# Kernel tuning notes

Hardware: AMD Instinct MI355X
Metric: run time of the kernel (lower is better)

## Reference

```python
import jax, jax.numpy as jnp
import numpy as np

NUM_CLASSES = 100
CLUSTERS_PER_CLASS = 64
LATENT_DIM = 128
BATCH = 32768


def setup_inputs() -> dict:
    key = jax.random.key(0)
    kx, kc, kl = jax.random.split(key, 3)
    x = jax.random.normal(kx, (BATCH, LATENT_DIM), dtype=jnp.float32)
    # nn.Parameter(torch.randn(C, Kc, D) * 0.1)
    centers = jax.random.normal(kc, (NUM_CLASSES, CLUSTERS_PER_CLASS, LATENT_DIM), dtype=jnp.float32) * 0.1
    labels = jax.random.randint(kl, (BATCH,), 0, NUM_CLASSES, dtype=jnp.int64)
    return {"x": x, "centers": centers, "labels": labels}


def reference(x, centers, labels):
    # [C, Kc, D] -> [K, D]
    all_centers = centers.reshape(-1, LATENT_DIM).astype(x.dtype)
    x2 = jnp.sum(x * x, axis=-1, keepdims=True)            # [B,1]
    c2 = jnp.sum(all_centers * all_centers, axis=-1)       # [K]
    sq = x2 + c2[None, :] - 2.0 * jnp.einsum('bd,kd->bk', x, all_centers)
    distances = jnp.sqrt(jnp.maximum(sq, 0.0))             # [B,K]
    closest_indices = jnp.argmin(distances, axis=1)        # [B]
    class_predictions = closest_indices // CLUSTERS_PER_CLASS
    cluster_assignments = closest_indices % CLUSTERS_PER_CLASS
    quantized_hard = all_centers[closest_indices]          # [B,D]
    min_distances = jnp.take_along_axis(distances, closest_indices[:, None], axis=1)[:, 0]
    # straight-through estimator (training path in the torch module)
    quantized = x + jax.lax.stop_gradient(quantized_hard - x)
    return quantized, cluster_assignments, min_distances, class_predictions
```

## Files before the change

kernel.cpp:

```cpp
#include <hip/hip_runtime.h>
#include <math.h>

#define BATCH  32768
#define D      128
#define K      6400
#define KC     64
#define ROWS_PER_BLOCK 64
#define CHUNK_C 128
#define NCHUNKS 50

typedef _Float16 half8 __attribute__((ext_vector_type(8)));
typedef float    floatx4 __attribute__((ext_vector_type(4)));

typedef __attribute__((address_space(3))) unsigned       lds_uint;
typedef __attribute__((address_space(1))) const unsigned glb_uint;

__device__ __forceinline__ void async_lds16(const void* g, void* l) {
    __builtin_amdgcn_global_load_lds((glb_uint*)g, (lds_uint*)l, 16, 0, 0);
}

__global__ __launch_bounds__(256) void pack_kernel(const float* __restrict__ centers,
                                                   _Float16* __restrict__ wh,
                                                   float* __restrict__ c2n) {
    int tid = blockIdx.x * 256 + threadIdx.x;
    int ch = tid >> 11;
    int u  = (tid >> 7) & 15;
    int cw = tid & 127;
    int center = ch * CHUNK_C + cw;
    const float* src = centers + (size_t)center * D + u * 8;
    float4 a = *(const float4*)src;
    float4 b = *(const float4*)(src + 4);
    float f[8] = {a.x, a.y, a.z, a.w, b.x, b.y, b.z, b.w};
    half8 h;
#pragma unroll
    for (int j = 0; j < 8; ++j) h[j] = (_Float16)f[j];
    *(half8*)(wh + (size_t)tid * 8) = h;

    if (blockIdx.x < K / KC) {
        int c_local = threadIdx.x >> 2, part = threadIdx.x & 3;
        int c = blockIdx.x * 64 + c_local;
        const float4* p = (const float4*)(centers + (size_t)c * D + part * 32);
        float s = 0.f;
#pragma unroll
        for (int i = 0; i < 8; ++i) {
            float4 v = p[i];
            s = fmaf(v.x, v.x, s); s = fmaf(v.y, v.y, s);
            s = fmaf(v.z, v.z, s); s = fmaf(v.w, v.w, s);
        }
        s += __shfl_xor(s, 1, 64);
        s += __shfl_xor(s, 2, 64);
        if (part == 0) c2n[c] = -0.5f * s;
    }
}

__global__ __launch_bounds__(512, 4) void dist_kernel(
    const float* __restrict__ x, const float* __restrict__ centers,
    const _Float16* __restrict__ wh, const float* __restrict__ c2n,
    float* __restrict__ out) {
    __shared__ char lds[65536];

    const int t    = threadIdx.x;
    const int w    = t >> 6;
    const int L    = t & 63;
    const int quad = L >> 4;
    const int n16  = L & 15;
    const int cq   = w & 3;
    const int rq   = w >> 2;
    const int gr0  = blockIdx.x * ROWS_PER_BLOCK;

    half8 Ah[2][4];
#pragma unroll
    for (int rt = 0; rt < 2; ++rt) {
        int r = gr0 + rq * 32 + rt * 16 + n16;
        const float* xr = x + (size_t)r * D + quad * 8;
#pragma unroll
        for (int ks = 0; ks < 4; ++ks) {
            float4 a = *(const float4*)(xr + ks * 32);
            float4 b = *(const float4*)(xr + ks * 32 + 4);
            float f[8] = {a.x, a.y, a.z, a.w, b.x, b.y, b.z, b.w};
            half8 h;
#pragma unroll
            for (int j = 0; j < 8; ++j) h[j] = (_Float16)f[j];
            Ah[rt][ks] = h;
        }
    }

    float b1[8], b2[8];
    int   j1_[8], j2_[8];
#pragma unroll
    for (int k = 0; k < 8; ++k) { b1[k] = -3.4e38f; b2[k] = -3.4e38f; j1_[k] = 0; j2_[k] = 0; }

    float pv[8]; int pi[8];
#pragma unroll
    for (int k = 0; k < 8; ++k) { pv[k] = -3.4e38f; pi[k] = 0; }

    const char* gh = (const char*)wh;

#pragma unroll
    for (int i = 0; i < 4; ++i) {
        int seg = w + i * 8;
        async_lds16(gh + seg * 1024 + L * 16, lds + seg * 1024);
    }

    float c2vA[2], c2vB[2];
#pragma unroll
    for (int ct = 0; ct < 2; ++ct) c2vA[ct] = c2n[cq * 32 + ct * 16 + n16];
    __syncthreads();

    for (int ci = 0; ci < NCHUNKS; ++ci) {
        const char* cur = lds + (ci & 1) * 32768;
        if (ci + 1 < NCHUNKS) {
            const char* gn = gh + (size_t)(ci + 1) * 32768;
            char* nxt = lds + ((ci + 1) & 1) * 32768;
#pragma unroll
            for (int i = 0; i < 4; ++i) {
                int seg = w + i * 8;
                async_lds16(gn + seg * 1024 + L * 16, nxt + seg * 1024);
            }
            const int kb1 = (ci + 1) * CHUNK_C + cq * 32;
#pragma unroll
            for (int ct = 0; ct < 2; ++ct) c2vB[ct] = c2n[kb1 + ct * 16 + n16];
        }

#pragma unroll
        for (int k = 0; k < 8; ++k) {
            float v = pv[k]; int vi = pi[k];
            bool bet1 = v > b1[k];
            bool bet2 = v > b2[k];
            float nb2 = bet1 ? b1[k] : (bet2 ? v : b2[k]);
            int   nj2 = bet1 ? j1_[k] : (bet2 ? vi : j2_[k]);
            b1[k]  = bet1 ? v : b1[k];
            j1_[k] = bet1 ? vi : j1_[k];
            b2[k]  = nb2;
            j2_[k] = nj2;
        }

        const int kbase = ci * CHUNK_C + cq * 32;

        floatx4 acc[2][2];
#pragma unroll
        for (int rt = 0; rt < 2; ++rt)
#pragma unroll
            for (int ct = 0; ct < 2; ++ct)
                acc[rt][ct] = (floatx4){c2vA[ct], c2vA[ct], c2vA[ct], c2vA[ct]};

        __builtin_amdgcn_s_setprio(1);
#pragma unroll
        for (int ks = 0; ks < 4; ++ks) {
            const half8* pb = (const half8*)cur + (ks * 4 + quad) * 128 + cq * 32 + n16;
#pragma unroll
            for (int ct = 0; ct < 2; ++ct) {
                half8 Bf = pb[ct * 16];
                acc[0][ct] = __builtin_amdgcn_mfma_f32_16x16x32_f16(Ah[0][ks], Bf, acc[0][ct], 0, 0, 0);
                acc[1][ct] = __builtin_amdgcn_mfma_f32_16x16x32_f16(Ah[1][ks], Bf, acc[1][ct], 0, 0, 0);
            }
        }
        __builtin_amdgcn_s_setprio(0);

        int i0 = kbase + n16;
#pragma unroll
        for (int rt = 0; rt < 2; ++rt)
#pragma unroll
            for (int reg = 0; reg < 4; ++reg) {
                float s0 = acc[rt][0][reg], s1 = acc[rt][1][reg];
                bool g01 = s1 > s0;
                int k = rt * 4 + reg;
                pv[k] = g01 ? s1 : s0;
                pi[k] = g01 ? i0 + 16 : i0;
            }

#pragma unroll
        for (int ct = 0; ct < 2; ++ct) c2vA[ct] = c2vB[ct];

        __syncthreads();
    }

#pragma unroll
    for (int k = 0; k < 8; ++k) {
        float v = pv[k]; int vi = pi[k];
        bool bet1 = v > b1[k];
        bool bet2 = v > b2[k];
        float nb2 = bet1 ? b1[k] : (bet2 ? v : b2[k]);
        int   nj2 = bet1 ? j1_[k] : (bet2 ? vi : j2_[k]);
        b1[k]  = bet1 ? v : b1[k];
        j1_[k] = bet1 ? vi : j1_[k];
        b2[k]  = nb2;
        j2_[k] = nj2;
    }

    int* candL = (int*)lds;

#pragma unroll
    for (int k = 0; k < 8; ++k) {
        float v1 = b1[k], v2 = b2[k];
        int   p1 = j1_[k], p2 = j2_[k];
#pragma unroll
        for (int m = 1; m < 16; m <<= 1) {
            float o1 = __shfl_xor(v1, m, 64), o2 = __shfl_xor(v2, m, 64);
            int   q1 = __shfl_xor(p1, m, 64), q2 = __shfl_xor(p2, m, 64);
            bool firstMine = (v1 > o1) || (v1 == o1 && p1 < q1);
            float nv1 = firstMine ? v1 : o1;  int np1 = firstMine ? p1 : q1;
            float cb  = firstMine ? o1 : v1;  int cpi = firstMine ? q1 : p1;
            float ob  = firstMine ? v2 : o2;  int obi = firstMine ? p2 : q2;
            bool secOwn = (ob > cb) || (ob == cb && obi < cpi);
            v1 = nv1; p1 = np1;
            v2 = secOwn ? ob : cb;  p2 = secOwn ? obi : cpi;
        }
        if (n16 == 0) {
            int rloc = rq * 32 + (k >> 2) * 16 + quad * 4 + (k & 3);
            candL[rloc * 8 + cq * 2 + 0] = p1;
            candL[rloc * 8 + cq * 2 + 1] = p2;
        }
    }
    __syncthreads();

    {
        int r = t >> 3, p = t & 7;
        int row = gr0 + r;
        int ix = candL[r * 8 + p];
        const float4* xr4 = (const float4*)(x + (size_t)row * D);
        const float4* c4  = (const float4*)(centers + (size_t)ix * D);
        float dot = 0.f, x2s = 0.f, c2 = 0.f;
#pragma unroll
        for (int d4 = 0; d4 < 32; ++d4) {
            float4 xv = xr4[d4], cv = c4[d4];
            dot = fmaf(xv.x, cv.x, dot); dot = fmaf(xv.y, cv.y, dot);
            dot = fmaf(xv.z, cv.z, dot); dot = fmaf(xv.w, cv.w, dot);
            x2s = fmaf(xv.x, xv.x, x2s); x2s = fmaf(xv.y, xv.y, x2s);
            x2s = fmaf(xv.z, xv.z, x2s); x2s = fmaf(xv.w, xv.w, x2s);
            c2  = fmaf(cv.x, cv.x, c2);  c2  = fmaf(cv.y, cv.y, c2);
            c2  = fmaf(cv.z, cv.z, c2);  c2  = fmaf(cv.w, cv.w, c2);
        }
        float sq = x2s + c2 - 2.f * dot;
#pragma unroll
        for (int m = 1; m < 8; m <<= 1) {
            float osq = __shfl_xor(sq, m, 64);
            int   oix = __shfl_xor(ix, m, 64);
            if (osq < sq || (osq == sq && oix < ix)) { sq = osq; ix = oix; }
        }

        float* out_clu = out + (size_t)BATCH * D;
        float* out_md  = out_clu + BATCH;
        float* out_cls = out_md + BATCH;
        if (p == 0) {
            out_md[row]  = sqrtf(fmaxf(sq, 0.f));
            out_clu[row] = (float)(ix & (KC - 1));
            out_cls[row] = (float)(ix >> 6);
        }

        const float4* cv4 = (const float4*)(centers + (size_t)ix * D) + p * 4;
        const float4* xv4 = (const float4*)(x + (size_t)row * D) + p * 4;
        float4* o4 = (float4*)(out + (size_t)row * D) + p * 4;
#pragma unroll
        for (int i = 0; i < 4; ++i) {
            float4 cv = cv4[i], xv = xv4[i];
            float4 o;
            o.x = xv.x + (cv.x - xv.x);
            o.y = xv.y + (cv.y - xv.y);
            o.z = xv.z + (cv.z - xv.z);
            o.w = xv.w + (cv.w - xv.w);
            o4[i] = o;
        }
    }
}

extern "C" void kernel_launch(void* const* d_in, const int* in_sizes, int n_in,
                              void* d_out, int out_size, void* d_ws, size_t ws_size,
                              hipStream_t stream) {
    const float* x       = (const float*)d_in[0];
    const float* centers = (const float*)d_in[1];
    float* out = (float*)d_out;

    _Float16* wh  = (_Float16*)d_ws;
    float*    c2n = (float*)(wh + (size_t)K * D);

    pack_kernel<<<(K * 16) / 256, 256, 0, stream>>>(centers, wh, c2n);
    dist_kernel<<<BATCH / ROWS_PER_BLOCK, 512, 0, stream>>>(x, centers, wh, c2n, out);
}
```

Before: 189.6 us.

## Load center fragments directly into registers, dropping LDS double buffer

Replaces the LDS double-buffered async global-to-LDS staging of packed fp16 centers with direct per-wave global loads into register double buffers (B0/B1), unrolled by two chunks. This removes the per-chunk __syncthreads and LDS traffic, and the launch bounds drop to 2 blocks per CU to make room for the extra registers. The cost is that each wave in a block loads the same center data separately through L1/L2 instead of sharing it via LDS, and occupancy is lower.

```diff
diff --git a/kernel.cpp b/kernel.cpp
--- a/kernel.cpp
+++ b/kernel.cpp
@@ -11,13 +11,6 @@
 
 typedef _Float16 half8 __attribute__((ext_vector_type(8)));
 typedef float    floatx4 __attribute__((ext_vector_type(4)));
-
-typedef __attribute__((address_space(3))) unsigned       lds_uint;
-typedef __attribute__((address_space(1))) const unsigned glb_uint;
-
-__device__ __forceinline__ void async_lds16(const void* g, void* l) {
-    __builtin_amdgcn_global_load_lds((glb_uint*)g, (lds_uint*)l, 16, 0, 0);
-}
 
 __global__ __launch_bounds__(256) void pack_kernel(const float* __restrict__ centers,
                                                    _Float16* __restrict__ wh,
@@ -53,11 +46,67 @@
     }
 }
 
-__global__ __launch_bounds__(512, 4) void dist_kernel(
+#define INSERT_PV()                                                         \
+    _Pragma("unroll")                                                       \
+    for (int k = 0; k < 8; ++k) {                                           \
+        float v = pv[k]; int vi = pi[k];                                    \
+        bool bet1 = v > b1[k];                                              \
+        bool bet2 = v > b2[k];                                              \
+        float nb2 = bet1 ? b1[k] : (bet2 ? v : b2[k]);                      \
+        int   nj2 = bet1 ? j1_[k] : (bet2 ? vi : j2_[k]);                   \
+        b1[k]  = bet1 ? v : b1[k];                                          \
+        j1_[k] = bet1 ? vi : j1_[k];                                        \
+        b2[k]  = nb2;                                                       \
+        j2_[k] = nj2;                                                       \
+    }
+
+#define COMPUTE_CHUNK(Bx, c2x, ci_)                                         \
+    {                                                                       \
+        floatx4 acc[2][2];                                                  \
+        _Pragma("unroll")                                                   \
+        for (int rt = 0; rt < 2; ++rt)                                      \
+            _Pragma("unroll")                                               \
+            for (int ct = 0; ct < 2; ++ct)                                  \
+                acc[rt][ct] = (floatx4){c2x[ct], c2x[ct], c2x[ct], c2x[ct]};\
+        _Pragma("unroll")                                                   \
+        for (int ks = 0; ks < 4; ++ks) {                                    \
+            _Pragma("unroll")                                               \
+            for (int ct = 0; ct < 2; ++ct) {                                \
+                half8 Bf = Bx[ks * 2 + ct];                                 \
+                acc[0][ct] = __builtin_amdgcn_mfma_f32_16x16x32_f16(Ah[0][ks], Bf, acc[0][ct], 0, 0, 0); \
+                acc[1][ct] = __builtin_amdgcn_mfma_f32_16x16x32_f16(Ah[1][ks], Bf, acc[1][ct], 0, 0, 0); \
+            }                                                               \
+        }                                                                   \
+        int i0 = (ci_) * CHUNK_C + cq * 32 + n16;                           \
+        _Pragma("unroll")                                                   \
+        for (int rt = 0; rt < 2; ++rt)                                      \
+            _Pragma("unroll")                                               \
+            for (int reg = 0; reg < 4; ++reg) {                             \
+                float s0 = acc[rt][0][reg], s1 = acc[rt][1][reg];           \
+                bool g01 = s1 > s0;                                         \
+                int k = rt * 4 + reg;                                       \
+                pv[k] = g01 ? s1 : s0;                                      \
+                pi[k] = g01 ? i0 + 16 : i0;                                 \
+            }                                                               \
+    }
+
+#define LOAD_B(Bx, ci_)                                                     \
+    _Pragma("unroll")                                                       \
+    for (int ks = 0; ks < 4; ++ks)                                          \
+        _Pragma("unroll")                                                   \
+        for (int ct = 0; ct < 2; ++ct)                                      \
+            Bx[ks * 2 + ct] = gB[(size_t)(ci_) * 2048 + ks * 512 + ct * 16];
+
+#define LOAD_C2(c2x, ci_)                                                   \
+    _Pragma("unroll")                                                       \
+    for (int ct = 0; ct < 2; ++ct)                                          \
+        c2x[ct] = c2n[(ci_) * CHUNK_C + cq * 32 + ct * 16 + n16];
+
+__global__ __launch_bounds__(512, 2) void dist_kernel(
     const float* __restrict__ x, const float* __restrict__ centers,
     const _Float16* __restrict__ wh, const float* __restrict__ c2n,
     float* __restrict__ out) {
-    __shared__ char lds[65536];
+    __shared__ int candL[ROWS_PER_BLOCK * 8];
 
     const int t    = threadIdx.x;
     const int w    = t >> 6;
@@ -94,101 +143,29 @@
 #pragma unroll
     for (int k = 0; k < 8; ++k) { pv[k] = -3.4e38f; pi[k] = 0; }
 
-    const char* gh = (const char*)wh;
-
-#pragma unroll
-    for (int i = 0; i < 4; ++i) {
-        int seg = w + i * 8;
-        async_lds16(gh + seg * 1024 + L * 16, lds + seg * 1024);
-    }
-
-    float c2vA[2], c2vB[2];
-#pragma unroll
-    for (int ct = 0; ct < 2; ++ct) c2vA[ct] = c2n[cq * 32 + ct * 16 + n16];
-    __syncthreads();
-
-    for (int ci = 0; ci < NCHUNKS; ++ci) {
-        const char* cur = lds + (ci & 1) * 32768;
-        if (ci + 1 < NCHUNKS) {
-            const char* gn = gh + (size_t)(ci + 1) * 32768;
-            char* nxt = lds + ((ci + 1) & 1) * 32768;
-#pragma unroll
-            for (int i = 0; i < 4; ++i) {
-                int seg = w + i * 8;
-                async_lds16(gn + seg * 1024 + L * 16, nxt + seg * 1024);
-            }
-            const int kb1 = (ci + 1) * CHUNK_C + cq * 32;
-#pragma unroll
-            for (int ct = 0; ct < 2; ++ct) c2vB[ct] = c2n[kb1 + ct * 16 + n16];
-        }
-
-#pragma unroll
-        for (int k = 0; k < 8; ++k) {
-            float v = pv[k]; int vi = pi[k];
-            bool bet1 = v > b1[k];
-            bool bet2 = v > b2[k];
-            float nb2 = bet1 ? b1[k] : (bet2 ? v : b2[k]);
-            int   nj2 = bet1 ? j1_[k] : (bet2 ? vi : j2_[k]);
-            b1[k]  = bet1 ? v : b1[k];
-            j1_[k] = bet1 ? vi : j1_[k];
-            b2[k]  = nb2;
-            j2_[k] = nj2;
-        }
-
-        const int kbase = ci * CHUNK_C + cq * 32;
-
-        floatx4 acc[2][2];
-#pragma unroll
-        for (int rt = 0; rt < 2; ++rt)
-#pragma unroll
-            for (int ct = 0; ct < 2; ++ct)
-                acc[rt][ct] = (floatx4){c2vA[ct], c2vA[ct], c2vA[ct], c2vA[ct]};
-
-        __builtin_amdgcn_s_setprio(1);
-#pragma unroll
-        for (int ks = 0; ks < 4; ++ks) {
-            const half8* pb = (const half8*)cur + (ks * 4 + quad) * 128 + cq * 32 + n16;
-#pragma unroll
-            for (int ct = 0; ct < 2; ++ct) {
-                half8 Bf = pb[ct * 16];
-                acc[0][ct] = __builtin_amdgcn_mfma_f32_16x16x32_f16(Ah[0][ks], Bf, acc[0][ct], 0, 0, 0);
-                acc[1][ct] = __builtin_amdgcn_mfma_f32_16x16x32_f16(Ah[1][ks], Bf, acc[1][ct], 0, 0, 0);
-            }
-        }
-        __builtin_amdgcn_s_setprio(0);
-
-        int i0 = kbase + n16;
-#pragma unroll
-        for (int rt = 0; rt < 2; ++rt)
-#pragma unroll
-            for (int reg = 0; reg < 4; ++reg) {
-                float s0 = acc[rt][0][reg], s1 = acc[rt][1][reg];
-                bool g01 = s1 > s0;
-                int k = rt * 4 + reg;
-                pv[k] = g01 ? s1 : s0;
-                pi[k] = g01 ? i0 + 16 : i0;
-            }
-
-#pragma unroll
-        for (int ct = 0; ct < 2; ++ct) c2vA[ct] = c2vB[ct];
-
-        __syncthreads();
-    }
-
-#pragma unroll
-    for (int k = 0; k < 8; ++k) {
-        float v = pv[k]; int vi = pi[k];
-        bool bet1 = v > b1[k];
-        bool bet2 = v > b2[k];
-        float nb2 = bet1 ? b1[k] : (bet2 ? v : b2[k]);
-        int   nj2 = bet1 ? j1_[k] : (bet2 ? vi : j2_[k]);
-        b1[k]  = bet1 ? v : b1[k];
-        j1_[k] = bet1 ? vi : j1_[k];
-        b2[k]  = nb2;
-        j2_[k] = nj2;
-    }
-
-    int* candL = (int*)lds;
+    const half8* gB = (const half8*)wh + quad * 128 + cq * 32 + n16;
+
+    half8 B0[8], B1[8];
+    float c2A[2], c2B[2];
+
+    LOAD_B(B0, 0)
+    LOAD_C2(c2A, 0)
+
+    for (int cc = 0; cc < NCHUNKS; cc += 2) {
+        LOAD_B(B1, cc + 1)
+        LOAD_C2(c2B, cc + 1)
+        INSERT_PV()
+        COMPUTE_CHUNK(B0, c2A, cc)
+
+        if (cc + 2 < NCHUNKS) {
+            LOAD_B(B0, cc + 2)
+            LOAD_C2(c2A, cc + 2)
+        }
+        INSERT_PV()
+        COMPUTE_CHUNK(B1, c2B, cc + 1)
+    }
+
+    INSERT_PV()
 
 #pragma unroll
     for (int k = 0; k < 8; ++k) {
```

New measurement: 191.3 us. No clear change (+0.9%).

## Halve rows per block, drop LDS double buffering to raise occupancy

Applied to the files above, without the earlier changes.

Each block now handles 32 rows instead of 64. The 64KB double-buffered center staging becomes a single 32KB buffer that is loaded and then synchronized at each chunk, and the launch bound asks for 8 blocks per CU. The pending-value register pipeline is dropped and the top-2 update is folded directly into the MFMA epilogue, which cuts register pressure. The aim is to hide memory latency through more resident blocks rather than in-block prefetch, at the cost of an exposed load and barrier per chunk and twice as many blocks re-reading the centers. The final straight-through write is also re-split so all 512 threads write coalesced row segments.

```diff
diff --git a/kernel.cpp b/kernel.cpp
--- a/kernel.cpp
+++ b/kernel.cpp
@@ -5,7 +5,7 @@
 #define D      128
 #define K      6400
 #define KC     64
-#define ROWS_PER_BLOCK 64
+#define ROWS_PER_BLOCK 32
 #define CHUNK_C 128
 #define NCHUNKS 50
 
@@ -53,11 +53,13 @@
     }
 }
 
-__global__ __launch_bounds__(512, 4) void dist_kernel(
+__global__ __launch_bounds__(512, 8) void dist_kernel(
     const float* __restrict__ x, const float* __restrict__ centers,
     const _Float16* __restrict__ wh, const float* __restrict__ c2n,
     float* __restrict__ out) {
-    __shared__ char lds[65536];
+    __shared__ char buf[32768];
+    __shared__ int  candL[ROWS_PER_BLOCK * 8];
+    __shared__ int  winIx[ROWS_PER_BLOCK];
 
     const int t    = threadIdx.x;
     const int w    = t >> 6;
@@ -68,10 +70,9 @@
     const int rq   = w >> 2;
     const int gr0  = blockIdx.x * ROWS_PER_BLOCK;
 
-    half8 Ah[2][4];
-#pragma unroll
-    for (int rt = 0; rt < 2; ++rt) {
-        int r = gr0 + rq * 32 + rt * 16 + n16;
+    half8 Ah[4];
+    {
+        int r = gr0 + rq * 16 + n16;
         const float* xr = x + (size_t)r * D + quad * 8;
 #pragma unroll
         for (int ks = 0; ks < 4; ++ks) {
@@ -81,93 +82,69 @@
             half8 h;
 #pragma unroll
             for (int j = 0; j < 8; ++j) h[j] = (_Float16)f[j];
-            Ah[rt][ks] = h;
-        }
-    }
-
-    float b1[8], b2[8];
-    int   j1_[8], j2_[8];
-#pragma unroll
-    for (int k = 0; k < 8; ++k) { b1[k] = -3.4e38f; b2[k] = -3.4e38f; j1_[k] = 0; j2_[k] = 0; }
-
-    float pv[8]; int pi[8];
-#pragma unroll
-    for (int k = 0; k < 8; ++k) { pv[k] = -3.4e38f; pi[k] = 0; }
+            Ah[ks] = h;
+        }
+    }
+
+    float b1[4], b2[4];
+    int   j1_[4], j2_[4];
+#pragma unroll
+    for (int k = 0; k < 4; ++k) { b1[k] = -3.4e38f; b2[k] = -3.4e38f; j1_[k] = 0; j2_[k] = 0; }
 
     const char* gh = (const char*)wh;
 
-#pragma unroll
-    for (int i = 0; i < 4; ++i) {
-        int seg = w + i * 8;
-        async_lds16(gh + seg * 1024 + L * 16, lds + seg * 1024);
-    }
-
     float c2vA[2], c2vB[2];
 #pragma unroll
     for (int ct = 0; ct < 2; ++ct) c2vA[ct] = c2n[cq * 32 + ct * 16 + n16];
-    __syncthreads();
 
     for (int ci = 0; ci < NCHUNKS; ++ci) {
-        const char* cur = lds + (ci & 1) * 32768;
+        const char* gsrc = gh + (size_t)ci * 32768;
+#pragma unroll
+        for (int i = 0; i < 4; ++i) {
+            int seg = w + i * 8;
+            async_lds16(gsrc + seg * 1024 + L * 16, buf + seg * 1024);
+        }
+        __syncthreads();
+
         if (ci + 1 < NCHUNKS) {
-            const char* gn = gh + (size_t)(ci + 1) * 32768;
-            char* nxt = lds + ((ci + 1) & 1) * 32768;
-#pragma unroll
-            for (int i = 0; i < 4; ++i) {
-                int seg = w + i * 8;
-                async_lds16(gn + seg * 1024 + L * 16, nxt + seg * 1024);
-            }
             const int kb1 = (ci + 1) * CHUNK_C + cq * 32;
 #pragma unroll
             for (int ct = 0; ct < 2; ++ct) c2vB[ct] = c2n[kb1 + ct * 16 + n16];
         }
 
-#pragma unroll
-        for (int k = 0; k < 8; ++k) {
-            float v = pv[k]; int vi = pi[k];
-            bool bet1 = v > b1[k];
-            bool bet2 = v > b2[k];
-            float nb2 = bet1 ? b1[k] : (bet2 ? v : b2[k]);
-            int   nj2 = bet1 ? j1_[k] : (bet2 ? vi : j2_[k]);
-            b1[k]  = bet1 ? v : b1[k];
-            j1_[k] = bet1 ? vi : j1_[k];
-            b2[k]  = nb2;
-            j2_[k] = nj2;
-        }
-
-        const int kbase = ci * CHUNK_C + cq * 32;
-
-        floatx4 acc[2][2];
-#pragma unroll
-        for (int rt = 0; rt < 2; ++rt)
-#pragma unroll
-            for (int ct = 0; ct < 2; ++ct)
-                acc[rt][ct] = (floatx4){c2vA[ct], c2vA[ct], c2vA[ct], c2vA[ct]};
+        floatx4 acc[2];
+#pragma unroll
+        for (int ct = 0; ct < 2; ++ct)
+            acc[ct] = (floatx4){c2vA[ct], c2vA[ct], c2vA[ct], c2vA[ct]};
 
         __builtin_amdgcn_s_setprio(1);
 #pragma unroll
         for (int ks = 0; ks < 4; ++ks) {
-            const half8* pb = (const half8*)cur + (ks * 4 + quad) * 128 + cq * 32 + n16;
+            const half8* pb = (const half8*)buf + (ks * 4 + quad) * 128 + cq * 32 + n16;
 #pragma unroll
             for (int ct = 0; ct < 2; ++ct) {
                 half8 Bf = pb[ct * 16];
-                acc[0][ct] = __builtin_amdgcn_mfma_f32_16x16x32_f16(Ah[0][ks], Bf, acc[0][ct], 0, 0, 0);
-                acc[1][ct] = __builtin_amdgcn_mfma_f32_16x16x32_f16(Ah[1][ks], Bf, acc[1][ct], 0, 0, 0);
+                acc[ct] = __builtin_amdgcn_mfma_f32_16x16x32_f16(Ah[ks], Bf, acc[ct], 0, 0, 0);
             }
         }
         __builtin_amdgcn_s_setprio(0);
 
-        int i0 = kbase + n16;
-#pragma unroll
-        for (int rt = 0; rt < 2; ++rt)
-#pragma unroll
-            for (int reg = 0; reg < 4; ++reg) {
-                float s0 = acc[rt][0][reg], s1 = acc[rt][1][reg];
-                bool g01 = s1 > s0;
-                int k = rt * 4 + reg;
-                pv[k] = g01 ? s1 : s0;
-                pi[k] = g01 ? i0 + 16 : i0;
-            }
+        int i0 = ci * CHUNK_C + cq * 32 + n16;
+#pragma unroll
+        for (int reg = 0; reg < 4; ++reg) {
+            float s0 = acc[0][reg], s1 = acc[1][reg];
+            bool g01 = s1 > s0;
+            float v  = g01 ? s1 : s0;
+            int   vi = g01 ? i0 + 16 : i0;
+            bool bet1 = v > b1[reg];
+            bool bet2 = v > b2[reg];
+            float nb2 = bet1 ? b1[reg] : (bet2 ? v : b2[reg]);
+            int   nj2 = bet1 ? j1_[reg] : (bet2 ? vi : j2_[reg]);
+            b1[reg]  = bet1 ? v : b1[reg];
+            j1_[reg] = bet1 ? vi : j1_[reg];
+            b2[reg]  = nb2;
+            j2_[reg] = nj2;
+        }
 
 #pragma unroll
         for (int ct = 0; ct < 2; ++ct) c2vA[ct] = c2vB[ct];
@@ -176,22 +153,7 @@
     }
 
 #pragma unroll
-    for (int k = 0; k < 8; ++k) {
-        float v = pv[k]; int vi = pi[k];
-        bool bet1 = v > b1[k];
-        bool bet2 = v > b2[k];
-        float nb2 = bet1 ? b1[k] : (bet2 ? v : b2[k]);
-        int   nj2 = bet1 ? j1_[k] : (bet2 ? vi : j2_[k]);
-        b1[k]  = bet1 ? v : b1[k];
-        j1_[k] = bet1 ? vi : j1_[k];
-        b2[k]  = nb2;
-        j2_[k] = nj2;
-    }
-
-    int* candL = (int*)lds;
-
-#pragma unroll
-    for (int k = 0; k < 8; ++k) {
+    for (int k = 0; k < 4; ++k) {
         float v1 = b1[k], v2 = b2[k];
         int   p1 = j1_[k], p2 = j2_[k];
 #pragma unroll
@@ -207,14 +169,14 @@
             v2 = secOwn ? ob : cb;  p2 = secOwn ? obi : cpi;
         }
         if (n16 == 0) {
-            int rloc = rq * 32 + (k >> 2) * 16 + quad * 4 + (k & 3);
+            int rloc = rq * 16 + quad * 4 + k;
             candL[rloc * 8 + cq * 2 + 0] = p1;
             candL[rloc * 8 + cq * 2 + 1] = p2;
         }
     }
     __syncthreads();
 
-    {
+    if (t < 256) {
         int r = t >> 3, p = t & 7;
         int row = gr0 + r;
         int ix = candL[r * 8 + p];
@@ -246,20 +208,28 @@
             out_md[row]  = sqrtf(fmaxf(sq, 0.f));
             out_clu[row] = (float)(ix & (KC - 1));
             out_cls[row] = (float)(ix >> 6);
-        }
-
-        const float4* cv4 = (const float4*)(centers + (size_t)ix * D) + p * 4;
-        const float4* xv4 = (const float4*)(x + (size_t)row * D) + p * 4;
-        float4* o4 = (float4*)(out + (size_t)row * D) + p * 4;
-#pragma unroll
-        for (int i = 0; i < 4; ++i) {
-            float4 cv = cv4[i], xv = xv4[i];
+            winIx[r] = ix;
+        }
+    }
+    __syncthreads();
+
+    {
+        int r = t >> 4, pq = t & 15;
+        int row = gr0 + r;
+        int ix = winIx[r];
+        const float4* cv4 = (const float4*)(centers + (size_t)ix * D);
+        const float4* xv4 = (const float4*)(x + (size_t)row * D);
+        float4* o4 = (float4*)(out + (size_t)row * D);
+#pragma unroll
+        for (int h = 0; h < 2; ++h) {
+            int d4 = pq + h * 16;
+            float4 cv = cv4[d4], xv = xv4[d4];
             float4 o;
             o.x = xv.x + (cv.x - xv.x);
             o.y = xv.y + (cv.y - xv.y);
             o.z = xv.z + (cv.z - xv.z);
             o.w = xv.w + (cv.w - xv.w);
-            o4[i] = o;
+            o4[d4] = o;
         }
     }
 }
```

Measured after the change: 203.3 us. +7.2%, slower.
